# Optimization experiments

Hardware: AMD Instinct MI355X
Metric: run time of the kernel (lower is better)

Reference implementation:

```python
import jax, jax.numpy as jnp
import numpy as np
from jax import lax

B_, L_, D_MODEL, D_FF = 8, 1024, 512, 2048
D_STATE, D_CONV, EXPAND = 16, 4, 2
D_IN = EXPAND * D_MODEL
DT_RANK = (D_MODEL + 15) // 16  # 32


def _ln(x, g, b, eps=1e-5):
    m = jnp.mean(x, -1, keepdims=True)
    v = jnp.var(x, -1, keepdims=True)
    return (x - m) / jnp.sqrt(v + eps) * g + b


def _selective_scan(u, dt, A, Bm, Cm, D):
    # u, dt: (B,L,d_in); Bm, Cm: (B,L,d_state); A: (d_in,d_state); D: (d_in,)
    def step(h, xs):
        dt_t, B_t, C_t, u_t = xs  # (B,d_in),(B,ds),(B,ds),(B,d_in)
        dA = jnp.exp(dt_t[..., None] * A)                       # (B,d_in,ds)
        h = dA * h + (dt_t * u_t)[..., None] * B_t[:, None, :]  # (B,d_in,ds)
        y = jnp.einsum('bds,bs->bd', h, C_t)
        return h, y

    h0 = jnp.zeros((u.shape[0], D_IN, D_STATE), u.dtype)
    xs = (dt.transpose(1, 0, 2), Bm.transpose(1, 0, 2),
          Cm.transpose(1, 0, 2), u.transpose(1, 0, 2))
    _, ys = lax.scan(step, h0, xs)           # (L,B,d_in)
    return ys.transpose(1, 0, 2) + u * D


def _mamba(x, in_w, conv_w, conv_b, xp_w, dtp_w, dtp_b, A_log, D, out_w):
    xz = x @ in_w.T                              # (B,L,2*d_in)
    xs, z = jnp.split(xz, 2, axis=-1)
    # causal depthwise conv1d over L
    xc = lax.conv_general_dilated(xs.transpose(0, 2, 1), conv_w, (1,),
                                  [(D_CONV - 1, 0)], feature_group_count=D_IN)
    xc = jax.nn.silu(xc + conv_b[None, :, None]).transpose(0, 2, 1)  # (B,L,d_in)
    x_dbl = xc @ xp_w.T
    dt, Bm, Cm = jnp.split(x_dbl, [DT_RANK, DT_RANK + D_STATE], axis=-1)
    dt = jax.nn.softplus(dt @ dtp_w.T + dtp_b)
    A = -jnp.exp(A_log)
    y = _selective_scan(xc, dt, A, Bm, Cm, D)
    y = y * jax.nn.silu(z)
    return y @ out_w.T


def _forward(x,
             in1_w, conv1d1_w, conv1d1_b, xp1_w, dtp1_w, dtp1_b, Alog1, D1, outp1_w,
             in2_w, conv1d2_w, conv1d2_b, xp2_w, dtp2_w, dtp2_b, Alog2, D2, outp2_w,
             c1_w, c1_b, c2_w, c2_b, ln1_g, ln1_b, ln2_g, ln2_b):
    x_res = x  # dropout is identity in eval
    fwd = _mamba(x, in1_w, conv1d1_w, conv1d1_b, xp1_w, dtp1_w, dtp1_b, Alog1, D1, outp1_w)
    bwd = _mamba(jnp.flip(x, 1), in2_w, conv1d2_w, conv1d2_b, xp2_w, dtp2_w, dtp2_b,
                 Alog2, D2, outp2_w)
    new_x = fwd + jnp.flip(bwd, 1)
    x = _ln(new_x + x_res, ln1_g, ln1_b)
    y = jax.nn.gelu(jnp.einsum('bld,fd->blf', x, c1_w[:, :, 0]) + c1_b, approximate=False)
    y = jnp.einsum('blf,df->bld', y, c2_w[:, :, 0]) + c2_b
    return _ln(x + y, ln2_g, ln2_b)


def setup_inputs() -> dict:
    key = jax.random.key(0)
    ks = iter(jax.random.split(key, 32))
    rn = lambda shape, s=0.02: jax.random.normal(next(ks), shape, jnp.float32) * s

    def mamba_params():
        return dict(in_w=rn((2 * D_IN, D_MODEL)), conv_w=rn((D_IN, 1, D_CONV)),
                    conv_b=rn((D_IN,)), xp_w=rn((DT_RANK + 2 * D_STATE, D_IN)),
                    dtp_w=rn((D_IN, DT_RANK)), dtp_b=rn((D_IN,)),
                    A_log=jnp.log(jnp.tile(jnp.arange(1., D_STATE + 1.), (D_IN, 1))).astype(jnp.float32),
                    D=jnp.ones((D_IN,), jnp.float32), out_w=rn((D_MODEL, D_IN)))

    m1, m2 = mamba_params(), mamba_params()
    return {
        'x': jax.random.normal(next(ks), (B_, L_, D_MODEL), jnp.float32),
        'in1_w': m1['in_w'], 'conv1d1_w': m1['conv_w'], 'conv1d1_b': m1['conv_b'],
        'xp1_w': m1['xp_w'], 'dtp1_w': m1['dtp_w'], 'dtp1_b': m1['dtp_b'],
        'Alog1': m1['A_log'], 'D1': m1['D'], 'outp1_w': m1['out_w'],
        'in2_w': m2['in_w'], 'conv1d2_w': m2['conv_w'], 'conv1d2_b': m2['conv_b'],
        'xp2_w': m2['xp_w'], 'dtp2_w': m2['dtp_w'], 'dtp2_b': m2['dtp_b'],
        'Alog2': m2['A_log'], 'D2': m2['D'], 'outp2_w': m2['out_w'],
        'c1_w': rn((D_FF, D_MODEL, 1)), 'c1_b': rn((D_FF,)),
        'c2_w': rn((D_MODEL, D_FF, 1)), 'c2_b': rn((D_MODEL,)),
        'ln1_g': jnp.ones((D_MODEL,), jnp.float32), 'ln1_b': jnp.zeros((D_MODEL,), jnp.float32),
        'ln2_g': jnp.ones((D_MODEL,), jnp.float32), 'ln2_b': jnp.zeros((D_MODEL,), jnp.float32),
    }


def reference(x,
              in1_w, conv1d1_w, conv1d1_b, xp1_w, dtp1_w, dtp1_b, Alog1, D1, outp1_w,
              in2_w, conv1d2_w, conv1d2_b, xp2_w, dtp2_w, dtp2_b, Alog2, D2, outp2_w,
              c1_w, c1_b, c2_w, c2_b, ln1_g, ln1_b, ln2_g, ln2_b):
    return _forward(x,
                    in1_w, conv1d1_w, conv1d1_b, xp1_w, dtp1_w, dtp1_b, Alog1, D1, outp1_w,
                    in2_w, conv1d2_w, conv1d2_b, xp2_w, dtp2_w, dtp2_b, Alog2, D2, outp2_w,
                    c1_w, c1_b, c2_w, c2_b, ln1_g, ln1_b, ln2_g, ln2_b)
```

## Files before the change

kernel.cpp:

```cpp
#include <hip/hip_runtime.h>
#include <hip/hip_bf16.h>
#include <math.h>

#define B_SZ 8
#define L_SZ 1024
#define DM 512
#define DFF 2048
#define DIN 1024
#define DSTATE 16
#define DTRANK 32
#define MROWS (B_SZ * L_SZ)
#define CH 256
#define NCH 4

typedef __hip_bfloat16 bf16;
typedef unsigned short u16;
using f32x4 = __attribute__((ext_vector_type(4))) float;
using bfrag = __attribute__((ext_vector_type(8))) short;

__device__ inline float ldf(const float* p, long i) { return p[i]; }
__device__ inline float ldf(const bf16* p, long i) {
  return __uint_as_float((unsigned)((const u16*)p)[i] << 16);
}
__device__ inline void stf(float* p, long i, float v) { p[i] = v; }
__device__ inline void stf(bf16* p, long i, float v) { p[i] = __float2bfloat16(v); }
__device__ inline float b2f(u16 x) {
  return __uint_as_float((unsigned)x << 16);
}
__device__ inline u16 f2b(float v) {
  union { bf16 h; u16 u; } c;
  c.h = __float2bfloat16(v);
  return c.u;
}

__device__ inline float fexp2(float x) {
  float r;
  asm("v_exp_f32 %0, %1" : "=v"(r) : "v"(x));
  return r;
}

typedef __attribute__((address_space(1))) const void g_void;
typedef __attribute__((address_space(3))) void l_void;
__device__ inline void gl_lds16(const void* g, void* l) {
  __builtin_amdgcn_global_load_lds((g_void*)g, (l_void*)l, 16, 0, 0);
}

__device__ inline float4 ld4f_bt(const float* p) { return *(const float4*)p; }
__device__ inline float4 ld4f_bt(const bf16* p) {
  ushort4 u = *(const ushort4*)p;
  float4 v;
  v.x = b2f(u.x); v.y = b2f(u.y); v.z = b2f(u.z); v.w = b2f(u.w);
  return v;
}

__device__ inline void ld16f(const float* p, uint4& lo, uint4& hi) {
  float4 a = *(const float4*)p, b = *(const float4*)(p + 4);
  float4 c = *(const float4*)(p + 8), d = *(const float4*)(p + 12);
  union { uint4 v; u16 s[8]; } L, H;
  L.s[0] = f2b(a.x); L.s[1] = f2b(a.y); L.s[2] = f2b(a.z); L.s[3] = f2b(a.w);
  L.s[4] = f2b(b.x); L.s[5] = f2b(b.y); L.s[6] = f2b(b.z); L.s[7] = f2b(b.w);
  H.s[0] = f2b(c.x); H.s[1] = f2b(c.y); H.s[2] = f2b(c.z); H.s[3] = f2b(c.w);
  H.s[4] = f2b(d.x); H.s[5] = f2b(d.y); H.s[6] = f2b(d.z); H.s[7] = f2b(d.w);
  lo = L.v; hi = H.v;
}

__device__ inline float dpp_add_r8(float x) {
  float r; asm("v_add_f32 %0, %1, %2 row_ror:8" : "=v"(r) : "v"(x), "v"(x)); return r;
}
__device__ inline float dpp_add_r4(float x) {
  float r; asm("v_add_f32 %0, %1, %2 row_ror:4" : "=v"(r) : "v"(x), "v"(x)); return r;
}
__device__ inline float dpp_add_r2(float x) {
  float r; asm("v_add_f32 %0, %1, %2 row_ror:2" : "=v"(r) : "v"(x), "v"(x)); return r;
}
__device__ inline float dpp_add_r1(float x) {
  float r; asm("v_add_f32 %0, %1, %2 row_ror:1" : "=v"(r) : "v"(x), "v"(x)); return r;
}
__device__ inline float row16_sum(float x) {
  return dpp_add_r1(dpp_add_r2(dpp_add_r4(dpp_add_r8(x))));
}

__global__ __launch_bounds__(256) void cvt_k(const float* __restrict__ s,
                                             bf16* __restrict__ d, int n) {
  int i = blockIdx.x * 256 + threadIdx.x;
  if (i < n) d[i] = __float2bfloat16(s[i]);
}

constexpr int MEPI_STORE_BF16 = 0;
constexpr int MEPI_GATE = 1;
constexpr int MEPI_BIAS_GELU = 2;
constexpr int MEPI_BIAS_RES = 3;

template <int EPI, bool FLIPA, typename TA, typename TO>
__global__ __launch_bounds__(256) void mgemm_k(
    const TA* __restrict__ Ab, int lda,
    const bf16* __restrict__ Wb, int ldw,
    TO* __restrict__ C, int ldc,
    const float* __restrict__ bias,
    const float* __restrict__ res,
    int K) {
  constexpr bool ABF = (sizeof(TA) == 2);
  __shared__ u16 Wsm[128][32];
  __shared__ u16 AsmL[128][32];
  __shared__ u16 AsmP[128][40];
  const int tid = threadIdx.x;
  const int m0 = blockIdx.y * 128;
  const int n0 = blockIdx.x * 128;

  const int srow4 = tid >> 2;
  const int q16 = tid & 3;
  const u16* Wg0 = (const u16*)Wb + (long)(n0 + srow4) * ldw + q16 * 8;
  const u16* Wg1 = (const u16*)Wb + (long)(n0 + 64 + srow4) * ldw + q16 * 8;
  char* WsmB = (char*)&Wsm[0][0] + (tid >> 6) * 1024;

  int ra0 = m0 + srow4, ra1 = m0 + 64 + srow4;
  if (FLIPA) {
    int t0 = ra0 & (L_SZ - 1); ra0 = (ra0 - t0) + (L_SZ - 1 - t0);
    int t1 = ra1 & (L_SZ - 1); ra1 = (ra1 - t1) + (L_SZ - 1 - t1);
  }
  const u16* Ag0 = (const u16*)Ab + (long)ra0 * lda + q16 * 8;
  const u16* Ag1 = (const u16*)Ab + (long)ra1 * lda + q16 * 8;
  char* AsmB = (char*)&AsmL[0][0] + (tid >> 6) * 1024;

  const int srow = tid >> 1;
  const int scol = (tid & 1) * 16;
  int arf = m0 + srow;
  if (FLIPA) { int t = arf & (L_SZ - 1); arf = (arf - t) + (L_SZ - 1 - t); }
  const TA* Agf = Ab + (long)arf * lda + scol;

  const int lane = tid & 63, quad = lane >> 4, l16 = lane & 15;
  const int wid = tid >> 6;
  const int wm = (wid & 1) * 64, wn = (wid >> 1) * 64;

  f32x4 acc[4][4];
#pragma unroll
  for (int i = 0; i < 4; ++i)
#pragma unroll
    for (int j = 0; j < 4; ++j) acc[i][j] = {0.f, 0.f, 0.f, 0.f};

  for (int k0 = 0; k0 < K; k0 += 32) {
    uint4 av0, av1;
    if (!ABF) ld16f((const float*)(Agf + k0), av0, av1);
    __syncthreads();
    gl_lds16(Wg0 + k0, WsmB);
    gl_lds16(Wg1 + k0, WsmB + 4096);
    if (ABF) {
      gl_lds16(Ag0 + k0, AsmB);
      gl_lds16(Ag1 + k0, AsmB + 4096);
    } else {
      *(uint4*)&AsmP[srow][scol] = av0;
      *(uint4*)&AsmP[srow][scol + 8] = av1;
    }
    __syncthreads();
    bfrag a[4], b[4];
#pragma unroll
    for (int mi = 0; mi < 4; ++mi)
      a[mi] = ABF ? *(const bfrag*)&AsmL[wm + mi * 16 + l16][quad * 8]
                  : *(const bfrag*)&AsmP[wm + mi * 16 + l16][quad * 8];
#pragma unroll
    for (int ni = 0; ni < 4; ++ni)
      b[ni] = *(const bfrag*)&Wsm[wn + ni * 16 + l16][quad * 8];
#pragma unroll
    for (int mi = 0; mi < 4; ++mi)
#pragma unroll
      for (int ni = 0; ni < 4; ++ni)
        acc[mi][ni] = __builtin_amdgcn_mfma_f32_16x16x32_bf16(
            a[mi], b[ni], acc[mi][ni], 0, 0, 0);
  }

#pragma unroll
  for (int mi = 0; mi < 4; ++mi)
#pragma unroll
    for (int ni = 0; ni < 4; ++ni)
#pragma unroll
      for (int r = 0; r < 4; ++r) {
        int row = m0 + wm + mi * 16 + quad * 4 + r;
        int col = n0 + wn + ni * 16 + l16;
        long oi = (long)row * ldc + col;
        float v = acc[mi][ni][r];
        if (EPI == MEPI_STORE_BF16) {
          stf(C, oi, v);
        } else if (EPI == MEPI_GATE) {
          float y = ldf((const bf16*)C, oi);
          float sz = v / (1.f + __expf(-v));
          stf(C, oi, y * sz);
        } else if (EPI == MEPI_BIAS_GELU) {
          v += bias[col];
          v = 0.5f * v * (1.f + erff(v * 0.70710678118654752440f));
          stf(C, oi, v);
        } else if (EPI == MEPI_BIAS_RES) {
          ((float*)C)[oi] = v + bias[col] + res[oi];
        }
      }
}

__global__ __launch_bounds__(256) void mmerge_k(
    const bf16* __restrict__ y1, const bf16* __restrict__ y2,
    const bf16* __restrict__ W1, const bf16* __restrict__ W2,
    const float* __restrict__ xres, float* __restrict__ newx) {
  __shared__ u16 AsmL[128][32];
  __shared__ u16 Wsm[128][32];
  const int tid = threadIdx.x;
  const int m0 = blockIdx.y * 128;
  const int n0 = blockIdx.x * 128;

  const int srow4 = tid >> 2;
  const int q16 = tid & 3;
  int r1a = m0 + srow4, r1b = m0 + 64 + srow4;
  int ta = r1a & (L_SZ - 1), tb = r1b & (L_SZ - 1);
  int r2a = (r1a - ta) + (L_SZ - 1 - ta);
  int r2b = (r1b - tb) + (L_SZ - 1 - tb);
  const u16* A1g0 = (const u16*)y1 + (long)r1a * DIN + q16 * 8;
  const u16* A1g1 = (const u16*)y1 + (long)r1b * DIN + q16 * 8;
  const u16* A2g0 = (const u16*)y2 + (long)r2a * DIN + q16 * 8;
  const u16* A2g1 = (const u16*)y2 + (long)r2b * DIN + q16 * 8;
  const u16* W1g0 = (const u16*)W1 + (long)(n0 + srow4) * DIN + q16 * 8;
  const u16* W1g1 = (const u16*)W1 + (long)(n0 + 64 + srow4) * DIN + q16 * 8;
  const u16* W2g0 = (const u16*)W2 + (long)(n0 + srow4) * DIN + q16 * 8;
  const u16* W2g1 = (const u16*)W2 + (long)(n0 + 64 + srow4) * DIN + q16 * 8;
  char* AsmB = (char*)&AsmL[0][0] + (tid >> 6) * 1024;
  char* WsmB = (char*)&Wsm[0][0] + (tid >> 6) * 1024;

  const int lane = tid & 63, quad = lane >> 4, l16 = lane & 15;
  const int wid = tid >> 6;
  const int wm = (wid & 1) * 64, wn = (wid >> 1) * 64;

  f32x4 acc[4][4];
#pragma unroll
  for (int i = 0; i < 4; ++i)
#pragma unroll
    for (int j = 0; j < 4; ++j) acc[i][j] = {0.f, 0.f, 0.f, 0.f};

  for (int k0 = 0; k0 < 2 * DIN; k0 += 32) {
    const bool ph2 = (k0 >= DIN);
    const int kk = k0 & (DIN - 1);
    const u16* a0 = ph2 ? A2g0 : A1g0;
    const u16* a1 = ph2 ? A2g1 : A1g1;
    const u16* w0 = ph2 ? W2g0 : W1g0;
    const u16* w1 = ph2 ? W2g1 : W1g1;
    __syncthreads();
    gl_lds16(a0 + kk, AsmB);
    gl_lds16(a1 + kk, AsmB + 4096);
    gl_lds16(w0 + kk, WsmB);
    gl_lds16(w1 + kk, WsmB + 4096);
    __syncthreads();
    bfrag a[4], b[4];
#pragma unroll
    for (int mi = 0; mi < 4; ++mi)
      a[mi] = *(const bfrag*)&AsmL[wm + mi * 16 + l16][quad * 8];
#pragma unroll
    for (int ni = 0; ni < 4; ++ni)
      b[ni] = *(const bfrag*)&Wsm[wn + ni * 16 + l16][quad * 8];
#pragma unroll
    for (int mi = 0; mi < 4; ++mi)
#pragma unroll
      for (int ni = 0; ni < 4; ++ni)
        acc[mi][ni] = __builtin_amdgcn_mfma_f32_16x16x32_bf16(
            a[mi], b[ni], acc[mi][ni], 0, 0, 0);
  }

#pragma unroll
  for (int mi = 0; mi < 4; ++mi)
#pragma unroll
    for (int ni = 0; ni < 4; ++ni)
#pragma unroll
      for (int r = 0; r < 4; ++r) {
        int row = m0 + wm + mi * 16 + quad * 4 + r;
        int col = n0 + wn + ni * 16 + l16;
        long oi = (long)row * DM + col;
        newx[oi] = acc[mi][ni][r] + xres[oi];
      }
}

constexpr int EPI_NONE = 0;
constexpr int EPI_SOFTPLUS_ROW = 1;

#define BM 64
#define BN 64
#define BKK 16

template <int EPI, typename TB, typename TO>
__global__ __launch_bounds__(256) void gemmBT_k(
    const float* __restrict__ A,
    const TB* __restrict__ B,
    TO* __restrict__ C, int N,
    const float* __restrict__ bias, int K) {
  __shared__ float As[BKK][BM + 4];
  __shared__ float Bs[BKK][BN + 4];
  const int tid = threadIdx.x;
  const int m0 = blockIdx.y * BM;
  const int n0 = blockIdx.x * BN;
  const int tx = tid & 15;
  const int ty = tid >> 4;
  const int lrow = tid >> 2;
  const int lcol = (tid & 3) * 4;
  const int kr = tid >> 4;
  const int nc = (tid & 15) * 4;

  const float* Arow = A + (long)(m0 + lrow) * K;

  float acc[4][4] = {};
  for (int k0 = 0; k0 < K; k0 += BKK) {
    float4 av = *(const float4*)(Arow + k0 + lcol);
    float4 bv = ld4f_bt(B + (long)(k0 + kr) * N + n0 + nc);
    As[lcol + 0][lrow] = av.x; As[lcol + 1][lrow] = av.y;
    As[lcol + 2][lrow] = av.z; As[lcol + 3][lrow] = av.w;
    Bs[kr][nc + 0] = bv.x; Bs[kr][nc + 1] = bv.y;
    Bs[kr][nc + 2] = bv.z; Bs[kr][nc + 3] = bv.w;
    __syncthreads();
#pragma unroll
    for (int k = 0; k < BKK; ++k) {
      float a[4], b[4];
#pragma unroll
      for (int i = 0; i < 4; ++i) a[i] = As[k][ty * 4 + i];
#pragma unroll
      for (int j = 0; j < 4; ++j) b[j] = Bs[k][tx * 4 + j];
#pragma unroll
      for (int i = 0; i < 4; ++i)
#pragma unroll
        for (int j = 0; j < 4; ++j) acc[i][j] += a[i] * b[j];
    }
    __syncthreads();
  }

#pragma unroll
  for (int i = 0; i < 4; ++i) {
    int r = m0 + ty * 4 + i;
#pragma unroll
    for (int j = 0; j < 4; ++j) {
      int c = n0 + tx * 4 + j;
      float v = acc[i][j];
      if (EPI == EPI_SOFTPLUS_ROW) {
        v += bias[r];
        v = (v > 20.f) ? v : log1pf(__expf(v));
      }
      stf(C, (long)r * N + c, v);
    }
  }
}

__global__ __launch_bounds__(256) void convT_k(
    const bf16* __restrict__ xs, const float* __restrict__ w,
    const float* __restrict__ b, bf16* __restrict__ xcT) {
  __shared__ u16 T[64][72];
  int c0 = blockIdx.x * 64;
  int r0 = blockIdx.y * 64;
  int tid = threadIdx.x;
  int tr = tid >> 2;
  int tc = (tid & 3) * 16;

  const u16* src = (const u16*)xs + (long)(r0 + tr) * DIN + c0 + tc;
  uint4 v0 = *(const uint4*)src;
  uint4 v1 = *(const uint4*)(src + 8);
  u16 tmp[16];
  *(uint4*)tmp = v0;
  *(uint4*)(tmp + 8) = v1;
#pragma unroll
  for (int j = 0; j < 16; ++j) T[tc + j][tr + 3] = tmp[j];
  bool head = (r0 & (L_SZ - 1)) == 0;
  if (tid < 12) {
    int hr = tid >> 2;
    int seg = (tid & 3) * 16;
    if (head) {
#pragma unroll
      for (int j = 0; j < 16; ++j) T[seg + j][hr] = 0;
    } else {
      const u16* hs = (const u16*)xs + (long)(r0 - 3 + hr) * DIN + c0 + seg;
      uint4 h0 = *(const uint4*)hs;
      uint4 h1 = *(const uint4*)(hs + 8);
      u16 ht[16];
      *(uint4*)ht = h0;
      *(uint4*)(ht + 8) = h1;
#pragma unroll
      for (int j = 0; j < 16; ++j) T[seg + j][hr] = ht[j];
    }
  }
  __syncthreads();

  int d = c0 + tr;
  float w0 = w[d * 4 + 0], w1 = w[d * 4 + 1], w2 = w[d * 4 + 2], w3 = w[d * 4 + 3];
  float bd = b[d];
  float X[19];
#pragma unroll
  for (int k = 0; k < 19; ++k) X[k] = b2f(T[tr][tc + k]);
  u16 o[16];
#pragma unroll
  for (int j = 0; j < 16; ++j) {
    float acc = bd + w0 * X[j] + w1 * X[j + 1] + w2 * X[j + 2] + w3 * X[j + 3];
    o[j] = f2b(acc / (1.f + __expf(-acc)));
  }
  u16* dst = (u16*)xcT + (long)d * MROWS + r0 + tc;
  *(uint4*)dst = *(uint4*)o;
  *(uint4*)(dst + 8) = *(uint4*)(o + 8);
}

__global__ __launch_bounds__(256, 4) void scan1_k(
    const u16* __restrict__ dtT1, const u16* __restrict__ dtT2,
    const u16* __restrict__ uT1, const u16* __restrict__ uT2,
    const float* __restrict__ xd1, const float* __restrict__ xd2,
    const float* __restrict__ Alog1, const float* __restrict__ Alog2,
    bf16* __restrict__ hl1, bf16* __restrict__ hl2,
    float* __restrict__ sd1, float* __restrict__ sd2) {
  int blk = blockIdx.x;
  int dblk = blk & 15;
  int r = blk >> 4;
  int c = r % 3; r /= 3;
  int b = r & 7;
  int dir = r >> 3;
  int tid = threadIdx.x;
  int s = tid & 15;
  int gi = tid >> 4;
  int d0 = dblk * 64 + gi * 4;
  const u16* dtT = dir ? dtT2 : dtT1;
  const u16* uT = dir ? uT2 : uT1;
  const float* xd = dir ? xd2 : xd1;
  const float* Alog = dir ? Alog2 : Alog1;
  bf16* hl = dir ? hl2 : hl1;
  float* sd = dir ? sd2 : sd1;

  float A2[4], h[4], sdt[4];
#pragma unroll
  for (int dd = 0; dd < 4; ++dd) {
    A2[dd] = -__expf(Alog[(d0 + dd) * DSTATE + s]) * 1.4426950408889634f;
    h[dd] = 0.f;
    sdt[dd] = 0.f;
  }
  long t0 = (long)b * L_SZ + c * CH;
  const u16* pdt = dtT + (long)d0 * MROWS + t0;
  const u16* pu = uT + (long)d0 * MROWS + t0;
  const float* pB = xd + (long)(DTRANK + s) * MROWS + t0;

  for (int g = 0; g < CH / 8; ++g) {
    union { uint4 v; u16 a[8]; } dt8[4], u8[4];
    union { float4 v[2]; float a[8]; } B8;
#pragma unroll
    for (int dd = 0; dd < 4; ++dd) {
      dt8[dd].v = *(const uint4*)(pdt + (long)dd * MROWS + g * 8);
      u8[dd].v = *(const uint4*)(pu + (long)dd * MROWS + g * 8);
    }
    B8.v[0] = *(const float4*)(pB + g * 8);
    B8.v[1] = *(const float4*)(pB + g * 8 + 4);
#pragma unroll
    for (int j = 0; j < 8; ++j) {
      float Bj = B8.a[j];
#pragma unroll
      for (int dd = 0; dd < 4; ++dd) {
        float dtv = b2f(dt8[dd].a[j]);
        float uv = b2f(u8[dd].a[j]);
        float da = fexp2(dtv * A2[dd]);
        h[dd] = da * h[dd] + (dtv * uv) * Bj;
        sdt[dd] += dtv;
      }
    }
  }
#pragma unroll
  for (int dd = 0; dd < 4; ++dd) {
    int ci = (b * 3 + c) * 1024 + d0 + dd;
    hl[(long)ci * 16 + s] = __float2bfloat16(h[dd]);
    if (s == 0) sd[ci] = sdt[dd];
  }
}

__global__ __launch_bounds__(256, 4) void scan2_k(
    const u16* __restrict__ dtT1, const u16* __restrict__ dtT2,
    const u16* __restrict__ uT1, const u16* __restrict__ uT2,
    const float* __restrict__ xd1, const float* __restrict__ xd2,
    const float* __restrict__ Alog1, const float* __restrict__ Alog2,
    const float* __restrict__ D1, const float* __restrict__ D2,
    const bf16* __restrict__ hl1, const bf16* __restrict__ hl2,
    const float* __restrict__ sd1, const float* __restrict__ sd2,
    bf16* __restrict__ y1, bf16* __restrict__ y2) {
  int blk = blockIdx.x;
  int dblk = blk & 15;
  int c = (blk >> 4) & 3;
  int b = (blk >> 6) & 7;
  int dir = blk >> 9;
  int tid = threadIdx.x;
  int s = tid & 15;
  int gi = tid >> 4;
  int d0 = dblk * 64 + gi * 4;
  const u16* dtT = dir ? dtT2 : dtT1;
  const u16* uT = dir ? uT2 : uT1;
  const float* xd = dir ? xd2 : xd1;
  const float* Alog = dir ? Alog2 : Alog1;
  const float* Dp = dir ? D2 : D1;
  const bf16* hl = dir ? hl2 : hl1;
  const float* sd = dir ? sd2 : sd1;
  bf16* out = dir ? y2 : y1;

  float A2[4], h[4], Dd[4];
#pragma unroll
  for (int dd = 0; dd < 4; ++dd) {
    A2[dd] = -__expf(Alog[(d0 + dd) * DSTATE + s]) * 1.4426950408889634f;
    Dd[dd] = Dp[d0 + dd];
    h[dd] = 0.f;
  }

  for (int cc = 0; cc < c; ++cc) {
#pragma unroll
    for (int dd = 0; dd < 4; ++dd) {
      int ci = (b * 3 + cc) * 1024 + d0 + dd;
      float P = fexp2(A2[dd] * sd[ci]);
      h[dd] = h[dd] * P + b2f(((const u16*)hl)[(long)ci * 16 + s]);
    }
  }

  long t0 = (long)b * L_SZ + c * CH;
  const u16* pdt = dtT + (long)d0 * MROWS + t0;
  const u16* pu = uT + (long)d0 * MROWS + t0;
  const float* pB = xd + (long)(DTRANK + s) * MROWS + t0;
  const float* pC = xd + (long)(DTRANK + DSTATE + s) * MROWS + t0;
  u16* outb = (u16*)out + (long)b * L_SZ * DIN + (long)c * CH * DIN + d0;

  for (int g = 0; g < CH / 8; ++g) {
    union { uint4 v; u16 a[8]; } dt8[4], u8[4];
    union { float4 v[2]; float a[8]; } B8, C8;
#pragma unroll
    for (int dd = 0; dd < 4; ++dd) {
      dt8[dd].v = *(const uint4*)(pdt + (long)dd * MROWS + g * 8);
      u8[dd].v = *(const uint4*)(pu + (long)dd * MROWS + g * 8);
    }
    B8.v[0] = *(const float4*)(pB + g * 8);
    B8.v[1] = *(const float4*)(pB + g * 8 + 4);
    C8.v[0] = *(const float4*)(pC + g * 8);
    C8.v[1] = *(const float4*)(pC + g * 8 + 4);
    u16* og = outb + (long)g * 8 * DIN;
#pragma unroll
    for (int j = 0; j < 8; ++j) {
      float Bj = B8.a[j];
      float Cj = C8.a[j];
      u16 o4[4];
#pragma unroll
      for (int dd = 0; dd < 4; ++dd) {
        float dtv = b2f(dt8[dd].a[j]);
        float uv = b2f(u8[dd].a[j]);
        float da = fexp2(dtv * A2[dd]);
        h[dd] = da * h[dd] + (dtv * uv) * Bj;
        float q = row16_sum(h[dd] * Cj);
        o4[dd] = f2b(q + Dd[dd] * uv);
      }
      if (s == 0) *(uint2*)(og + (long)j * DIN) = *(uint2*)o4;
    }
  }
}

__global__ __launch_bounds__(256) void ln_k(
    const float* __restrict__ xin, const float* __restrict__ g,
    const float* __restrict__ bb, float* __restrict__ out,
    bf16* __restrict__ outb) {
  int row = blockIdx.x;
  const float* p = xin + (long)row * DM;
  int tid = threadIdx.x;
  float x0 = p[tid], x1 = p[tid + 256];
  float sum = x0 + x1;
  float sq = x0 * x0 + x1 * x1;
#pragma unroll
  for (int o = 1; o < 64; o <<= 1) {
    sum += __shfl_xor(sum, o, 64);
    sq += __shfl_xor(sq, o, 64);
  }
  __shared__ float ssum[4], ssq[4];
  int wv = tid >> 6;
  if ((tid & 63) == 0) { ssum[wv] = sum; ssq[wv] = sq; }
  __syncthreads();
  sum = ssum[0] + ssum[1] + ssum[2] + ssum[3];
  sq = ssq[0] + ssq[1] + ssq[2] + ssq[3];
  float mean = sum * (1.f / DM);
  float var = sq * (1.f / DM) - mean * mean;
  float rstd = rsqrtf(var + 1e-5f);
  float v0 = (x0 - mean) * rstd * g[tid] + bb[tid];
  float v1 = (x1 - mean) * rstd * g[tid + 256] + bb[tid + 256];
  out[(long)row * DM + tid] = v0;
  out[(long)row * DM + tid + 256] = v1;
  if (outb) {
    stf(outb, (long)row * DM + tid, v0);
    stf(outb, (long)row * DM + tid + 256, v1);
  }
}

extern "C" void kernel_launch(void* const* d_in, const int* in_sizes, int n_in,
                              void* d_out, int out_size, void* d_ws, size_t ws_size,
                              hipStream_t stream) {
  const float* x = (const float*)d_in[0];
  const float* in1_w = (const float*)d_in[1];
  const float* conv1_w = (const float*)d_in[2];
  const float* conv1_b = (const float*)d_in[3];
  const float* xp1_w = (const float*)d_in[4];
  const float* dtp1_w = (const float*)d_in[5];
  const float* dtp1_b = (const float*)d_in[6];
  const float* Alog1 = (const float*)d_in[7];
  const float* D1 = (const float*)d_in[8];
  const float* outp1_w = (const float*)d_in[9];
  const float* in2_w = (const float*)d_in[10];
  const float* conv2_w = (const float*)d_in[11];
  const float* conv2_b = (const float*)d_in[12];
  const float* xp2_w = (const float*)d_in[13];
  const float* dtp2_w = (const float*)d_in[14];
  const float* dtp2_b = (const float*)d_in[15];
  const float* Alog2 = (const float*)d_in[16];
  const float* D2 = (const float*)d_in[17];
  const float* outp2_w = (const float*)d_in[18];
  const float* c1_w = (const float*)d_in[19];
  const float* c1_b = (const float*)d_in[20];
  const float* c2_w = (const float*)d_in[21];
  const float* c2_b = (const float*)d_in[22];
  const float* ln1_g = (const float*)d_in[23];
  const float* ln1_b = (const float*)d_in[24];
  const float* ln2_g = (const float*)d_in[25];
  const float* ln2_b = (const float*)d_in[26];

  const long MB = 1024L * 1024;
  char* wsb = (char*)d_ws;
  bf16* A = (bf16*)(wsb + 0 * MB);
  bf16* B = (bf16*)(wsb + 16 * MB);
  bf16* C = (bf16*)(wsb + 32 * MB);
  bf16* D = (bf16*)(wsb + 48 * MB);
  bf16* E = (bf16*)(wsb + 64 * MB);
  bf16* F = (bf16*)(wsb + 80 * MB);
  float* Bf = (float*)B;
  float* Cf = (float*)C;
  float* Af = (float*)A;
  bf16* ffn = C;

  char* ob = (char*)d_out;
  bf16* in1b = (bf16*)(ob + 0 * MB);
  bf16* in2b = (bf16*)(ob + 2 * MB);
  bf16* o1b = (bf16*)(ob + 4 * MB);
  bf16* o2b = (bf16*)(ob + 5 * MB);
  bf16* c1b = (bf16*)(ob + 6 * MB);
  bf16* c2b = (bf16*)(ob + 8 * MB);
  float* xdT1 = (float*)(ob + 10 * MB);
  float* xdT2 = (float*)(ob + 12 * MB);
  float* sd1 = (float*)(ob + 0);
  float* sd2 = (float*)(ob + 512 * 1024);
  bf16* hl1 = (bf16*)(ob + 14 * MB);
  bf16* hl2 = (bf16*)(ob + 15 * MB);

  dim3 blk(256);
  dim3 gP(DIN / 128, MROWS / 128);
  dim3 gM(DM / 128, MROWS / 128);
  dim3 gF(DFF / 128, MROWS / 128);
  dim3 gC(DIN / 64, MROWS / 64);
  dim3 gX(MROWS / BN, 64 / BM);
  dim3 gD(MROWS / BN, DIN / BM);

  cvt_k<<<(2 * DIN * DM) / 256, blk, 0, stream>>>(in1_w, in1b, 2 * DIN * DM);
  cvt_k<<<(2 * DIN * DM) / 256, blk, 0, stream>>>(in2_w, in2b, 2 * DIN * DM);
  cvt_k<<<(DM * DIN) / 256, blk, 0, stream>>>(outp1_w, o1b, DM * DIN);
  cvt_k<<<(DM * DIN) / 256, blk, 0, stream>>>(outp2_w, o2b, DM * DIN);
  cvt_k<<<(DFF * DM) / 256, blk, 0, stream>>>(c1_w, c1b, DFF * DM);
  cvt_k<<<(DM * DFF) / 256, blk, 0, stream>>>(c2_w, c2b, DM * DFF);

  mgemm_k<MEPI_STORE_BF16, false, float, bf16><<<gP, blk, 0, stream>>>(
      x, DM, in1b, DM, A, DIN, nullptr, nullptr, DM);
  convT_k<<<gC, blk, 0, stream>>>(A, conv1_w, conv1_b, B);
  gemmBT_k<EPI_NONE, bf16, float><<<gX, blk, 0, stream>>>(
      xp1_w, B, xdT1, MROWS, nullptr, DIN);
  gemmBT_k<EPI_SOFTPLUS_ROW, float, bf16><<<gD, blk, 0, stream>>>(
      dtp1_w, xdT1, C, MROWS, dtp1_b, DTRANK);

  mgemm_k<MEPI_STORE_BF16, true, float, bf16><<<gP, blk, 0, stream>>>(
      x, DM, in2b, DM, D, DIN, nullptr, nullptr, DM);
  convT_k<<<gC, blk, 0, stream>>>(D, conv2_w, conv2_b, E);
  gemmBT_k<EPI_NONE, bf16, float><<<gX, blk, 0, stream>>>(
      xp2_w, E, xdT2, MROWS, nullptr, DIN);
  gemmBT_k<EPI_SOFTPLUS_ROW, float, bf16><<<gD, blk, 0, stream>>>(
      dtp2_w, xdT2, F, MROWS, dtp2_b, DTRANK);

  scan1_k<<<2 * 8 * 3 * 16, blk, 0, stream>>>(
      (const u16*)C, (const u16*)F, (const u16*)B, (const u16*)E,
      xdT1, xdT2, Alog1, Alog2, hl1, hl2, sd1, sd2);
  scan2_k<<<2 * 8 * 4 * 16, blk, 0, stream>>>(
      (const u16*)C, (const u16*)F, (const u16*)B, (const u16*)E,
      xdT1, xdT2, Alog1, Alog2, D1, D2, hl1, hl2, sd1, sd2, A, D);

  mgemm_k<MEPI_GATE, false, float, bf16><<<gP, blk, 0, stream>>>(
      x, DM, in1b + (long)DIN * DM, DM, A, DIN, nullptr, nullptr, DM);
  mgemm_k<MEPI_GATE, true, float, bf16><<<gP, blk, 0, stream>>>(
      x, DM, in2b + (long)DIN * DM, DM, D, DIN, nullptr, nullptr, DM);

  mmerge_k<<<gM, blk, 0, stream>>>(A, D, o1b, o2b, x, Cf);

  ln_k<<<MROWS, blk, 0, stream>>>(Cf, ln1_g, ln1_b, Bf, E);

  mgemm_k<MEPI_BIAS_GELU, false, bf16, bf16><<<gF, blk, 0, stream>>>(
      E, DM, c1b, DM, ffn, DFF, c1_b, nullptr, DM);
  mgemm_k<MEPI_BIAS_RES, false, bf16, float><<<gM, blk, 0, stream>>>(
      ffn, DFF, c2b, DFF, Af, DM, c2_b, Bf, DFF);

  ln_k<<<MROWS, blk, 0, stream>>>(Af, ln2_g, ln2_b, (float*)d_out, nullptr);
}
```

Before: 812.7 us.

## Batch forward and backward in-projection GEMMs and merge weight conversions into one launch

The six weight-conversion launches become a single multi-segment conversion kernel. The forward and backward Mamba in-projection GEMMs (x-stream and gate) now each run as one GEMM over concatenated weights. Instead of flipping the A rows for the backward branch, the epilogue writes the second half of the output columns to a time-flipped row of a second buffer. This cuts kernel launches and reuses the shared A tile (x) across both directions. The cost is scattered flipped stores and a reshuffled workspace layout for sd/hl.

```diff
diff --git a/kernel.cpp b/kernel.cpp
--- a/kernel.cpp
+++ b/kernel.cpp
@@ -80,29 +80,47 @@
   return dpp_add_r1(dpp_add_r2(dpp_add_r4(dpp_add_r8(x))));
 }
 
-__global__ __launch_bounds__(256) void cvt_k(const float* __restrict__ s,
-                                             bf16* __restrict__ d, int n) {
-  int i = blockIdx.x * 256 + threadIdx.x;
-  if (i < n) d[i] = __float2bfloat16(s[i]);
-}
-
-constexpr int MEPI_STORE_BF16 = 0;
-constexpr int MEPI_GATE = 1;
+__device__ inline int flipL(int r) {
+  int t = r & (L_SZ - 1);
+  return (r - t) + (L_SZ - 1 - t);
+}
+
+__global__ __launch_bounds__(256) void cvt8_k(
+    const float* s0, const float* s1, const float* s2, const float* s3,
+    const float* s4, const float* s5, const float* s6, const float* s7,
+    bf16* d0, bf16* d1, bf16* d2, bf16* d3,
+    bf16* d4, bf16* d5, bf16* d6, bf16* d7) {
+  int blk = blockIdx.x;
+  const float* s; bf16* d; long off;
+  if (blk < 2048)       { s = s0; d = d0; off = (long)blk * 256; }
+  else if (blk < 4096)  { s = s1; d = d1; off = (long)(blk - 2048) * 256; }
+  else if (blk < 6144)  { s = s2; d = d2; off = (long)(blk - 4096) * 256; }
+  else if (blk < 8192)  { s = s3; d = d3; off = (long)(blk - 6144) * 256; }
+  else if (blk < 10240) { s = s4; d = d4; off = (long)(blk - 8192) * 256; }
+  else if (blk < 12288) { s = s5; d = d5; off = (long)(blk - 10240) * 256; }
+  else if (blk < 16384) { s = s6; d = d6; off = (long)(blk - 12288) * 256; }
+  else                  { s = s7; d = d7; off = (long)(blk - 16384) * 256; }
+  off += threadIdx.x;
+  d[off] = __float2bfloat16(s[off]);
+}
+
+constexpr int MEPI_STORE2 = 0;
+constexpr int MEPI_GATE2 = 1;
 constexpr int MEPI_BIAS_GELU = 2;
 constexpr int MEPI_BIAS_RES = 3;
 
-template <int EPI, bool FLIPA, typename TA, typename TO>
+template <int EPI, typename TA, typename TO>
 __global__ __launch_bounds__(256) void mgemm_k(
     const TA* __restrict__ Ab, int lda,
     const bf16* __restrict__ Wb, int ldw,
-    TO* __restrict__ C, int ldc,
+    TO* __restrict__ C, TO* __restrict__ C2, int ldc,
     const float* __restrict__ bias,
     const float* __restrict__ res,
     int K) {
   constexpr bool ABF = (sizeof(TA) == 2);
   __shared__ u16 Wsm[128][32];
-  __shared__ u16 AsmL[128][32];
-  __shared__ u16 AsmP[128][40];
+  __shared__ u16 AsmL[ABF ? 128 : 1][32];
+  __shared__ u16 AsmP[ABF ? 1 : 128][ABF ? 1 : 40];
   const int tid = threadIdx.x;
   const int m0 = blockIdx.y * 128;
   const int n0 = blockIdx.x * 128;
@@ -113,20 +131,13 @@
   const u16* Wg1 = (const u16*)Wb + (long)(n0 + 64 + srow4) * ldw + q16 * 8;
   char* WsmB = (char*)&Wsm[0][0] + (tid >> 6) * 1024;
 
-  int ra0 = m0 + srow4, ra1 = m0 + 64 + srow4;
-  if (FLIPA) {
-    int t0 = ra0 & (L_SZ - 1); ra0 = (ra0 - t0) + (L_SZ - 1 - t0);
-    int t1 = ra1 & (L_SZ - 1); ra1 = (ra1 - t1) + (L_SZ - 1 - t1);
-  }
-  const u16* Ag0 = (const u16*)Ab + (long)ra0 * lda + q16 * 8;
-  const u16* Ag1 = (const u16*)Ab + (long)ra1 * lda + q16 * 8;
+  const u16* Ag0 = (const u16*)Ab + (long)(m0 + srow4) * lda + q16 * 8;
+  const u16* Ag1 = (const u16*)Ab + (long)(m0 + 64 + srow4) * lda + q16 * 8;
   char* AsmB = (char*)&AsmL[0][0] + (tid >> 6) * 1024;
 
   const int srow = tid >> 1;
   const int scol = (tid & 1) * 16;
-  int arf = m0 + srow;
-  if (FLIPA) { int t = arf & (L_SZ - 1); arf = (arf - t) + (L_SZ - 1 - t); }
-  const TA* Agf = Ab + (long)arf * lda + scol;
+  const TA* Agf = Ab + (long)(m0 + srow) * lda + scol;
 
   const int lane = tid & 63, quad = lane >> 4, l16 = lane & 15;
   const int wid = tid >> 6;
@@ -140,11 +151,11 @@
 
   for (int k0 = 0; k0 < K; k0 += 32) {
     uint4 av0, av1;
-    if (!ABF) ld16f((const float*)(Agf + k0), av0, av1);
+    if constexpr (!ABF) ld16f((const float*)(Agf + k0), av0, av1);
     __syncthreads();
     gl_lds16(Wg0 + k0, WsmB);
     gl_lds16(Wg1 + k0, WsmB + 4096);
-    if (ABF) {
+    if constexpr (ABF) {
       gl_lds16(Ag0 + k0, AsmB);
       gl_lds16(Ag1 + k0, AsmB + 4096);
     } else {
@@ -154,9 +165,12 @@
     __syncthreads();
     bfrag a[4], b[4];
 #pragma unroll
-    for (int mi = 0; mi < 4; ++mi)
-      a[mi] = ABF ? *(const bfrag*)&AsmL[wm + mi * 16 + l16][quad * 8]
-                  : *(const bfrag*)&AsmP[wm + mi * 16 + l16][quad * 8];
+    for (int mi = 0; mi < 4; ++mi) {
+      if constexpr (ABF)
+        a[mi] = *(const bfrag*)&AsmL[wm + mi * 16 + l16][quad * 8];
+      else
+        a[mi] = *(const bfrag*)&AsmP[wm + mi * 16 + l16][quad * 8];
+    }
 #pragma unroll
     for (int ni = 0; ni < 4; ++ni)
       b[ni] = *(const bfrag*)&Wsm[wn + ni * 16 + l16][quad * 8];
@@ -168,6 +182,7 @@
             a[mi], b[ni], acc[mi][ni], 0, 0, 0);
   }
 
+  const bool second = (n0 >= DIN);
 #pragma unroll
   for (int mi = 0; mi < 4; ++mi)
 #pragma unroll
@@ -176,19 +191,24 @@
       for (int r = 0; r < 4; ++r) {
         int row = m0 + wm + mi * 16 + quad * 4 + r;
         int col = n0 + wn + ni * 16 + l16;
-        long oi = (long)row * ldc + col;
         float v = acc[mi][ni][r];
-        if (EPI == MEPI_STORE_BF16) {
-          stf(C, oi, v);
-        } else if (EPI == MEPI_GATE) {
-          float y = ldf((const bf16*)C, oi);
+        if (EPI == MEPI_STORE2) {
+          if (second) stf(C2, (long)flipL(row) * ldc + (col - DIN), v);
+          else stf(C, (long)row * ldc + col, v);
+        } else if (EPI == MEPI_GATE2) {
+          TO* T = second ? C2 : C;
+          long oi = second ? ((long)flipL(row) * ldc + (col - DIN))
+                           : ((long)row * ldc + col);
+          float y = ldf((const bf16*)T, oi);
           float sz = v / (1.f + __expf(-v));
-          stf(C, oi, y * sz);
+          stf(T, oi, y * sz);
         } else if (EPI == MEPI_BIAS_GELU) {
+          long oi = (long)row * ldc + col;
           v += bias[col];
           v = 0.5f * v * (1.f + erff(v * 0.70710678118654752440f));
           stf(C, oi, v);
         } else if (EPI == MEPI_BIAS_RES) {
+          long oi = (long)row * ldc + col;
           ((float*)C)[oi] = v + bias[col] + res[oi];
         }
       }
@@ -207,9 +227,7 @@
   const int srow4 = tid >> 2;
   const int q16 = tid & 3;
   int r1a = m0 + srow4, r1b = m0 + 64 + srow4;
-  int ta = r1a & (L_SZ - 1), tb = r1b & (L_SZ - 1);
-  int r2a = (r1a - ta) + (L_SZ - 1 - ta);
-  int r2b = (r1b - tb) + (L_SZ - 1 - tb);
+  int r2a = flipL(r1a), r2b = flipL(r1b);
   const u16* A1g0 = (const u16*)y1 + (long)r1a * DIN + q16 * 8;
   const u16* A1g1 = (const u16*)y1 + (long)r1b * DIN + q16 * 8;
   const u16* A2g0 = (const u16*)y2 + (long)r2a * DIN + q16 * 8;
@@ -623,45 +641,43 @@
   bf16* ffn = C;
 
   char* ob = (char*)d_out;
-  bf16* in1b = (bf16*)(ob + 0 * MB);
-  bf16* in2b = (bf16*)(ob + 2 * MB);
+  bf16* Wxs = (bf16*)(ob + 0 * MB);
+  bf16* Wg = (bf16*)(ob + 2 * MB);
   bf16* o1b = (bf16*)(ob + 4 * MB);
   bf16* o2b = (bf16*)(ob + 5 * MB);
   bf16* c1b = (bf16*)(ob + 6 * MB);
   bf16* c2b = (bf16*)(ob + 8 * MB);
   float* xdT1 = (float*)(ob + 10 * MB);
   float* xdT2 = (float*)(ob + 12 * MB);
-  float* sd1 = (float*)(ob + 0);
-  float* sd2 = (float*)(ob + 512 * 1024);
-  bf16* hl1 = (bf16*)(ob + 14 * MB);
+  float* sd1 = (float*)(ob + 14 * MB);
+  float* sd2 = (float*)(ob + 14 * MB + 131072);
+  bf16* hl1 = (bf16*)(ob + 14 * MB + 262144);
   bf16* hl2 = (bf16*)(ob + 15 * MB);
 
+  const long HWN = (long)DIN * DM;
+
   dim3 blk(256);
-  dim3 gP(DIN / 128, MROWS / 128);
+  dim3 gP2(2 * DIN / 128, MROWS / 128);
   dim3 gM(DM / 128, MROWS / 128);
   dim3 gF(DFF / 128, MROWS / 128);
   dim3 gC(DIN / 64, MROWS / 64);
   dim3 gX(MROWS / BN, 64 / BM);
   dim3 gD(MROWS / BN, DIN / BM);
 
-  cvt_k<<<(2 * DIN * DM) / 256, blk, 0, stream>>>(in1_w, in1b, 2 * DIN * DM);
-  cvt_k<<<(2 * DIN * DM) / 256, blk, 0, stream>>>(in2_w, in2b, 2 * DIN * DM);
-  cvt_k<<<(DM * DIN) / 256, blk, 0, stream>>>(outp1_w, o1b, DM * DIN);
-  cvt_k<<<(DM * DIN) / 256, blk, 0, stream>>>(outp2_w, o2b, DM * DIN);
-  cvt_k<<<(DFF * DM) / 256, blk, 0, stream>>>(c1_w, c1b, DFF * DM);
-  cvt_k<<<(DM * DFF) / 256, blk, 0, stream>>>(c2_w, c2b, DM * DFF);
-
-  mgemm_k<MEPI_STORE_BF16, false, float, bf16><<<gP, blk, 0, stream>>>(
-      x, DM, in1b, DM, A, DIN, nullptr, nullptr, DM);
+  cvt8_k<<<20480, blk, 0, stream>>>(
+      in1_w, in2_w, in1_w + HWN, in2_w + HWN, outp1_w, outp2_w, c1_w, c2_w,
+      Wxs, Wxs + HWN, Wg, Wg + HWN, o1b, o2b, c1b, c2b);
+
+  mgemm_k<MEPI_STORE2, float, bf16><<<gP2, blk, 0, stream>>>(
+      x, DM, Wxs, DM, A, D, DIN, nullptr, nullptr, DM);
+
   convT_k<<<gC, blk, 0, stream>>>(A, conv1_w, conv1_b, B);
+  convT_k<<<gC, blk, 0, stream>>>(D, conv2_w, conv2_b, E);
+
   gemmBT_k<EPI_NONE, bf16, float><<<gX, blk, 0, stream>>>(
       xp1_w, B, xdT1, MROWS, nullptr, DIN);
   gemmBT_k<EPI_SOFTPLUS_ROW, float, bf16><<<gD, blk, 0, stream>>>(
       dtp1_w, xdT1, C, MROWS, dtp1_b, DTRANK);
-
-  mgemm_k<MEPI_STORE_BF16, true, float, bf16><<<gP, blk, 0, stream>>>(
-      x, DM, in2b, DM, D, DIN, nullptr, nullptr, DM);
-  convT_k<<<gC, blk, 0, stream>>>(D, conv2_w, conv2_b, E);
   gemmBT_k<EPI_NONE, bf16, float><<<gX, blk, 0, stream>>>(
       xp2_w, E, xdT2, MROWS, nullptr, DIN);
   gemmBT_k<EPI_SOFTPLUS_ROW, float, bf16><<<gD, blk, 0, stream>>>(
@@ -674,19 +690,17 @@
       (const u16*)C, (const u16*)F, (const u16*)B, (const u16*)E,
       xdT1, xdT2, Alog1, Alog2, D1, D2, hl1, hl2, sd1, sd2, A, D);
 
-  mgemm_k<MEPI_GATE, false, float, bf16><<<gP, blk, 0, stream>>>(
-      x, DM, in1b + (long)DIN * DM, DM, A, DIN, nullptr, nullptr, DM);
-  mgemm_k<MEPI_GATE, true, float, bf16><<<gP, blk, 0, stream>>>(
-      x, DM, in2b + (long)DIN * DM, DM, D, DIN, nullptr, nullptr, DM);
+  mgemm_k<MEPI_GATE2, float, bf16><<<gP2, blk, 0, stream>>>(
+      x, DM, Wg, DM, A, D, DIN, nullptr, nullptr, DM);
 
   mmerge_k<<<gM, blk, 0, stream>>>(A, D, o1b, o2b, x, Cf);
 
   ln_k<<<MROWS, blk, 0, stream>>>(Cf, ln1_g, ln1_b, Bf, E);
 
-  mgemm_k<MEPI_BIAS_GELU, false, bf16, bf16><<<gF, blk, 0, stream>>>(
-      E, DM, c1b, DM, ffn, DFF, c1_b, nullptr, DM);
-  mgemm_k<MEPI_BIAS_RES, false, bf16, float><<<gM, blk, 0, stream>>>(
-      ffn, DFF, c2b, DFF, Af, DM, c2_b, Bf, DFF);
+  mgemm_k<MEPI_BIAS_GELU, bf16, bf16><<<gF, blk, 0, stream>>>(
+      E, DM, c1b, DM, ffn, nullptr, DFF, c1_b, nullptr, DM);
+  mgemm_k<MEPI_BIAS_RES, bf16, float><<<gM, blk, 0, stream>>>(
+      ffn, DFF, c2b, DFF, Af, nullptr, DM, c2_b, Bf, DFF);
 
   ln_k<<<MROWS, blk, 0, stream>>>(Af, ln2_g, ln2_b, (float*)d_out, nullptr);
 }
```

Result: no change. 800.4 us (-1.5%).
